# Performance work log

Hardware: AMD Instinct MI355X
Metric: run time of the kernel (lower is better)

## Reference

```python
import jax, jax.numpy as jnp
import numpy as np

N_NODES = 50000
N_EDGES = 1000000
D_IN = 64
D_OUT = 64
EDGE_DIM = 16
NEG_SLOPE = 0.2


def setup_inputs() -> dict:
    key = jax.random.key(0)
    ks = jax.random.split(key, 10)
    x = jax.random.normal(ks[0], (N_NODES, D_IN), dtype=jnp.float32)
    edge_index = jax.random.randint(ks[1], (2, N_EDGES), 0, N_NODES, dtype=jnp.int64)
    edge_attr = jax.random.normal(ks[2], (N_EDGES, EDGE_DIM), dtype=jnp.float32)
    s = 0.1
    W_l = jax.random.normal(ks[3], (D_IN, D_OUT), dtype=jnp.float32) * s
    b_l = jnp.zeros((D_OUT,), dtype=jnp.float32)
    W_r = jax.random.normal(ks[4], (D_IN, D_OUT), dtype=jnp.float32) * s
    b_r = jnp.zeros((D_OUT,), dtype=jnp.float32)
    W_e = jax.random.normal(ks[5], (EDGE_DIM, D_OUT), dtype=jnp.float32) * s
    att = jax.random.normal(ks[6], (D_OUT,), dtype=jnp.float32) * s
    bias = jnp.zeros((D_OUT,), dtype=jnp.float32)
    return {"x": x, "edge_index": edge_index, "edge_attr": edge_attr,
            "W_l": W_l, "b_l": b_l, "W_r": W_r, "b_r": b_r,
            "W_e": W_e, "att": att, "bias": bias}


def reference(x, edge_index, edge_attr, W_l, b_l, W_r, b_r, W_e, att, bias):
    # GATv2Conv (heads=1, concat) with edge features, share_weights=False.
    src = edge_index[0]  # message source j
    dst = edge_index[1]  # aggregation target i
    n = x.shape[0]

    x_l = x @ W_l + b_l          # [N, C] source transform
    x_r = x @ W_r + b_r          # [N, C] target transform
    e = edge_attr @ W_e          # [E, C] edge transform (no bias in lin_edge)

    # per-edge GATv2 attention logit: a^T LeakyReLU(x_l[j] + x_r[i] + e)
    h = jax.nn.leaky_relu(x_l[src] + x_r[dst] + e, NEG_SLOPE)  # [E, C]
    logits = h @ att  # [E]

    # segment softmax over incoming edges of each target node
    m = jax.ops.segment_max(logits, dst, num_segments=n)        # [N]
    ex = jnp.exp(logits - m[dst])                               # [E]
    denom = jax.ops.segment_sum(ex, dst, num_segments=n)       # [N]
    alpha = ex / (denom[dst] + 1e-16)                           # [E]

    # weighted scatter-add of source messages x_l[j]
    out = jax.ops.segment_sum(alpha[:, None] * x_l[src], dst, num_segments=n)
    return out + bias
```

## Files before the change

### kernel.cpp

```cpp
#include <hip/hip_runtime.h>
#include <hip/hip_bf16.h>
#include <math.h>

#define N_NODES 50000
#define N_EDGES 1000000
#define D 64
#define ED 16
#define NEG 0.2f

__device__ __forceinline__ float wave_sum(float v) {
  #pragma unroll
  for (int m = 32; m >= 1; m >>= 1) v += __shfl_xor(v, m, 64);
  return v;
}

__global__ void k_init(int* __restrict__ cursor) {
  int i = blockIdx.x * 256 + threadIdx.x;
  if (i < N_NODES) cursor[i] = 0;
}

__global__ __launch_bounds__(256) void k_transform(
    const float* __restrict__ x,
    const float* __restrict__ Wl, const float* __restrict__ bl,
    const float* __restrict__ Wr, const float* __restrict__ br,
    __hip_bfloat16* __restrict__ xlb, float* __restrict__ xr) {
  __shared__ float sW[2 * D * D];
  float* sWl = sW;
  float* sWr = sW + D * D;
  int t = threadIdx.x;
  for (int q = t; q < D * D / 4; q += 256) {
    ((float4*)sWl)[q] = ((const float4*)Wl)[q];
    ((float4*)sWr)[q] = ((const float4*)Wr)[q];
  }
  __syncthreads();
  int lane = t & 63;
  int row = blockIdx.x * 4 + (t >> 6);
  if (row >= N_NODES) return;
  float xv = x[row * D + lane];
  float accl = bl[lane], accr = br[lane];
  #pragma unroll
  for (int k = 0; k < D; k++) {
    float xk = __shfl(xv, k, 64);
    accl = fmaf(xk, sWl[k * D + lane], accl);
    accr = fmaf(xk, sWr[k * D + lane], accr);
  }
  xlb[row * D + lane] = __float2bfloat16(accl);
  xr[row * D + lane] = accr;
}

__global__ void k_hist(const int* __restrict__ ei, int* __restrict__ cursor) {
  int e = blockIdx.x * 256 + threadIdx.x;
  if (e < N_EDGES) atomicAdd(&cursor[ei[N_EDGES + e]], 1);
}

__global__ void k_scan_a(const int* __restrict__ counts, int* __restrict__ row_start,
                         int* __restrict__ bsum) {
  __shared__ int sb[256];
  int t = threadIdx.x;
  int i = blockIdx.x * 256 + t;
  int v = (i < N_NODES) ? counts[i] : 0;
  sb[t] = v;
  __syncthreads();
  for (int off = 1; off < 256; off <<= 1) {
    int add = (t >= off) ? sb[t - off] : 0;
    __syncthreads();
    sb[t] += add;
    __syncthreads();
  }
  if (i < N_NODES) row_start[i] = sb[t] - v;
  if (t == 255) bsum[blockIdx.x] = sb[t];
}
__global__ void k_scan_b(int* __restrict__ bsum, int nb) {
  __shared__ int sb[256];
  int t = threadIdx.x;
  int v = (t < nb) ? bsum[t] : 0;
  sb[t] = v;
  __syncthreads();
  for (int off = 1; off < 256; off <<= 1) {
    int add = (t >= off) ? sb[t - off] : 0;
    __syncthreads();
    sb[t] += add;
    __syncthreads();
  }
  if (t < nb) bsum[t] = sb[t] - v;
}
__global__ void k_scan_c(int* __restrict__ row_start, const int* __restrict__ bsum,
                         int* __restrict__ cursor) {
  int t = threadIdx.x;
  int i = blockIdx.x * 256 + t;
  if (i < N_NODES) {
    int r = row_start[i] + bsum[blockIdx.x];
    row_start[i] = r;
    cursor[i] = r;
  }
  if (i == 0) row_start[N_NODES] = N_EDGES;
}

__global__ void k_scatter(const int* __restrict__ ei, int* __restrict__ cursor,
                          int2* __restrict__ perm) {
  int e = blockIdx.x * 256 + threadIdx.x;
  if (e >= N_EDGES) return;
  int s = ei[e];
  int d = ei[N_EDGES + e];
  int pos = atomicAdd(&cursor[d], 1);
  perm[pos] = make_int2(e, s);
}

__global__ __launch_bounds__(256) void k_fused(
    const float* __restrict__ ea, const float* __restrict__ We,
    const float* __restrict__ att,
    const __hip_bfloat16* __restrict__ xlb, const float* __restrict__ xr,
    const int* __restrict__ row_start, const int2* __restrict__ perm,
    const float* __restrict__ bias, float* __restrict__ out) {
  __shared__ float sWe[ED * D];
  __shared__ float satt[D];
  int t = threadIdx.x;
  for (int q = t; q < ED * D / 4; q += 256) ((float4*)sWe)[q] = ((const float4*)We)[q];
  if (t < D) satt[t] = att[t];
  __syncthreads();
  int lane = t & 63;
  int n = blockIdx.x * 4 + (t >> 6);
  if (n >= N_NODES) return;
  int start = row_start[n];
  int end = row_start[n + 1];

  float xrv = xr[(size_t)n * D + lane];
  float av = satt[lane];
  float m = -INFINITY, lsum = 0.f, O = 0.f;

  const unsigned short* xlr16 = (const unsigned short*)xlb;

  if (start < end) {
    int2 p0 = perm[start];
    int e0 = __builtin_amdgcn_readfirstlane(p0.x);
    int s0 = __builtin_amdgcn_readfirstlane(p0.y);
    unsigned short xlr = xlr16[(size_t)s0 * D + lane];
    float eav = (lane < ED) ? ea[(size_t)e0 * ED + lane] : 0.f;
    int i1 = (start + 1 < end) ? start + 1 : start;
    int2 pp = perm[i1];

    for (int i = start; i < end; ++i) {
      int e_n = __builtin_amdgcn_readfirstlane(pp.x);
      int s_n = __builtin_amdgcn_readfirstlane(pp.y);
      unsigned short xlr_n = xlr16[(size_t)s_n * D + lane];
      float eav_n = (lane < ED) ? ea[(size_t)e_n * ED + lane] : 0.f;
      int i2 = (i + 2 < end) ? i + 2 : i1;
      pp = perm[i2];

      float xlv = __uint_as_float(((unsigned)xlr) << 16);
      float acc = 0.f;
      #pragma unroll
      for (int k = 0; k < ED; k++) {
        float ek = __shfl(eav, k, 64);
        acc = fmaf(ek, sWe[k * D + lane], acc);
      }
      float h = xlv + xrv + acc;
      h = (h > 0.f) ? h : NEG * h;
      float logit = wave_sum(h * av);
      float mn = fmaxf(m, logit);
      float sc = __expf(m - mn);
      float p = __expf(logit - mn);
      lsum = fmaf(lsum, sc, p);
      O = O * sc + p * xlv;
      m = mn;
      xlr = xlr_n;
      eav = eav_n;
    }
  }
  out[(size_t)n * D + lane] = O / (lsum + 1e-16f) + bias[lane];
}

static inline char* align_up(char* p, size_t a) {
  return (char*)(((uintptr_t)p + a - 1) & ~(uintptr_t)(a - 1));
}

extern "C" void kernel_launch(void* const* d_in, const int* in_sizes, int n_in,
                              void* d_out, int out_size, void* d_ws, size_t ws_size,
                              hipStream_t stream) {
  const float* x   = (const float*)d_in[0];
  const int* ei    = (const int*)d_in[1];
  const float* ea  = (const float*)d_in[2];
  const float* Wl  = (const float*)d_in[3];
  const float* bl  = (const float*)d_in[4];
  const float* Wr  = (const float*)d_in[5];
  const float* br  = (const float*)d_in[6];
  const float* We  = (const float*)d_in[7];
  const float* att = (const float*)d_in[8];
  const float* bias = (const float*)d_in[9];
  float* out = (float*)d_out;

  char* w = (char*)d_ws;
  __hip_bfloat16* xlb = (__hip_bfloat16*)w; w = align_up(w + (size_t)N_NODES * D * 2, 256);
  float* xr       = (float*)w; w = align_up(w + (size_t)N_NODES * D * 4, 256);
  int* row_start  = (int*)w;   w = align_up(w + (size_t)(N_NODES + 1) * 4, 256);
  int* cursor     = (int*)w;   w = align_up(w + (size_t)N_NODES * 4, 256);
  int* bsum       = (int*)w;   w = align_up(w + 256 * 4, 256);
  int2* perm      = (int2*)w;  w = align_up(w + (size_t)N_EDGES * 8, 256);

  const int NB = (N_NODES + 255) / 256;

  k_init<<<NB, 256, 0, stream>>>(cursor);
  k_transform<<<N_NODES / 4, 256, 0, stream>>>(x, Wl, bl, Wr, br, xlb, xr);
  k_hist<<<(N_EDGES + 255) / 256, 256, 0, stream>>>(ei, cursor);
  k_scan_a<<<NB, 256, 0, stream>>>(cursor, row_start, bsum);
  k_scan_b<<<1, 256, 0, stream>>>(bsum, NB);
  k_scan_c<<<NB, 256, 0, stream>>>(row_start, bsum, cursor);
  k_scatter<<<(N_EDGES + 255) / 256, 256, 0, stream>>>(ei, cursor, perm);
  k_fused<<<(N_NODES + 3) / 4, 256, 0, stream>>>(ea, We, att, xlb, xr, row_start,
                                                 perm, bias, out);
}
```

Before: 537.4 us.

## Pre-permute edge attributes into CSR order as bf16 during scatter

The scatter kernel now reads each edge's 16 float attributes and writes them as bf16 into dst-sorted CSR order alongside a source-only permutation array. The fused kernel then reads edge attributes contiguously instead of gathering random 64-byte rows by edge id, and reads only 4-byte source indices. This removes random gathers from the main aggregation loop in exchange for an extra 32MB write plus read, and bf16 rounding of edge attributes. The init kernel is also replaced by hipMemsetAsync.

```diff
diff --git a/kernel.cpp b/kernel.cpp
--- a/kernel.cpp
+++ b/kernel.cpp
@@ -14,9 +14,12 @@
   return v;
 }
 
-__global__ void k_init(int* __restrict__ cursor) {
-  int i = blockIdx.x * 256 + threadIdx.x;
-  if (i < N_NODES) cursor[i] = 0;
+__device__ __forceinline__ unsigned short f2bf(float x) {
+  __hip_bfloat16 h = __float2bfloat16(x);
+  return *(unsigned short*)&h;
+}
+__device__ __forceinline__ float bf2f(unsigned short u) {
+  return __uint_as_float(((unsigned)u) << 16);
 }
 
 __global__ __launch_bounds__(256) void k_transform(
@@ -97,20 +100,37 @@
 }
 
 __global__ void k_scatter(const int* __restrict__ ei, int* __restrict__ cursor,
-                          int2* __restrict__ perm) {
+                          int* __restrict__ src_perm, uint4* __restrict__ eap,
+                          const float* __restrict__ ea) {
   int e = blockIdx.x * 256 + threadIdx.x;
   if (e >= N_EDGES) return;
   int s = ei[e];
   int d = ei[N_EDGES + e];
+  const float4* ea4 = (const float4*)ea;
+  float4 a = ea4[(size_t)e * 4 + 0];
+  float4 b = ea4[(size_t)e * 4 + 1];
+  float4 c = ea4[(size_t)e * 4 + 2];
+  float4 f = ea4[(size_t)e * 4 + 3];
   int pos = atomicAdd(&cursor[d], 1);
-  perm[pos] = make_int2(e, s);
+  src_perm[pos] = s;
+  uint4 w0, w1;
+  w0.x = (unsigned)f2bf(a.x) | ((unsigned)f2bf(a.y) << 16);
+  w0.y = (unsigned)f2bf(a.z) | ((unsigned)f2bf(a.w) << 16);
+  w0.z = (unsigned)f2bf(b.x) | ((unsigned)f2bf(b.y) << 16);
+  w0.w = (unsigned)f2bf(b.z) | ((unsigned)f2bf(b.w) << 16);
+  w1.x = (unsigned)f2bf(c.x) | ((unsigned)f2bf(c.y) << 16);
+  w1.y = (unsigned)f2bf(c.z) | ((unsigned)f2bf(c.w) << 16);
+  w1.z = (unsigned)f2bf(f.x) | ((unsigned)f2bf(f.y) << 16);
+  w1.w = (unsigned)f2bf(f.z) | ((unsigned)f2bf(f.w) << 16);
+  eap[(size_t)pos * 2 + 0] = w0;
+  eap[(size_t)pos * 2 + 1] = w1;
 }
 
 __global__ __launch_bounds__(256) void k_fused(
-    const float* __restrict__ ea, const float* __restrict__ We,
+    const unsigned short* __restrict__ eap, const float* __restrict__ We,
     const float* __restrict__ att,
     const __hip_bfloat16* __restrict__ xlb, const float* __restrict__ xr,
-    const int* __restrict__ row_start, const int2* __restrict__ perm,
+    const int* __restrict__ row_start, const int* __restrict__ src_perm,
     const float* __restrict__ bias, float* __restrict__ out) {
   __shared__ float sWe[ED * D];
   __shared__ float satt[D];
@@ -131,27 +151,26 @@
   const unsigned short* xlr16 = (const unsigned short*)xlb;
 
   if (start < end) {
-    int2 p0 = perm[start];
-    int e0 = __builtin_amdgcn_readfirstlane(p0.x);
-    int s0 = __builtin_amdgcn_readfirstlane(p0.y);
+    int s0 = __builtin_amdgcn_readfirstlane(src_perm[start]);
     unsigned short xlr = xlr16[(size_t)s0 * D + lane];
-    float eav = (lane < ED) ? ea[(size_t)e0 * ED + lane] : 0.f;
+    unsigned short ear = (lane < ED) ? eap[(size_t)start * ED + lane] : 0;
     int i1 = (start + 1 < end) ? start + 1 : start;
-    int2 pp = perm[i1];
+    int sp = src_perm[i1];
 
     for (int i = start; i < end; ++i) {
-      int e_n = __builtin_amdgcn_readfirstlane(pp.x);
-      int s_n = __builtin_amdgcn_readfirstlane(pp.y);
+      int s_n = __builtin_amdgcn_readfirstlane(sp);
       unsigned short xlr_n = xlr16[(size_t)s_n * D + lane];
-      float eav_n = (lane < ED) ? ea[(size_t)e_n * ED + lane] : 0.f;
+      int inext = (i + 1 < end) ? i + 1 : i;
+      unsigned short ear_n = (lane < ED) ? eap[(size_t)inext * ED + lane] : 0;
       int i2 = (i + 2 < end) ? i + 2 : i1;
-      pp = perm[i2];
-
-      float xlv = __uint_as_float(((unsigned)xlr) << 16);
+      sp = src_perm[i2];
+
+      float xlv = bf2f(xlr);
+      float eavf = bf2f(ear);
       float acc = 0.f;
       #pragma unroll
       for (int k = 0; k < ED; k++) {
-        float ek = __shfl(eav, k, 64);
+        float ek = __shfl(eavf, k, 64);
         acc = fmaf(ek, sWe[k * D + lane], acc);
       }
       float h = xlv + xrv + acc;
@@ -164,7 +183,7 @@
       O = O * sc + p * xlv;
       m = mn;
       xlr = xlr_n;
-      eav = eav_n;
+      ear = ear_n;
     }
   }
   out[(size_t)n * D + lane] = O / (lsum + 1e-16f) + bias[lane];
@@ -195,17 +214,18 @@
   int* row_start  = (int*)w;   w = align_up(w + (size_t)(N_NODES + 1) * 4, 256);
   int* cursor     = (int*)w;   w = align_up(w + (size_t)N_NODES * 4, 256);
   int* bsum       = (int*)w;   w = align_up(w + 256 * 4, 256);
-  int2* perm      = (int2*)w;  w = align_up(w + (size_t)N_EDGES * 8, 256);
+  int* src_perm   = (int*)w;   w = align_up(w + (size_t)N_EDGES * 4, 256);
+  uint4* eap      = (uint4*)w; w = align_up(w + (size_t)N_EDGES * ED * 2, 256);
 
   const int NB = (N_NODES + 255) / 256;
 
-  k_init<<<NB, 256, 0, stream>>>(cursor);
+  hipMemsetAsync(cursor, 0, (size_t)N_NODES * 4, stream);
   k_transform<<<N_NODES / 4, 256, 0, stream>>>(x, Wl, bl, Wr, br, xlb, xr);
   k_hist<<<(N_EDGES + 255) / 256, 256, 0, stream>>>(ei, cursor);
   k_scan_a<<<NB, 256, 0, stream>>>(cursor, row_start, bsum);
   k_scan_b<<<1, 256, 0, stream>>>(bsum, NB);
   k_scan_c<<<NB, 256, 0, stream>>>(row_start, bsum, cursor);
-  k_scatter<<<(N_EDGES + 255) / 256, 256, 0, stream>>>(ei, cursor, perm);
-  k_fused<<<(N_NODES + 3) / 4, 256, 0, stream>>>(ea, We, att, xlb, xr, row_start,
-                                                 perm, bias, out);
-}
+  k_scatter<<<(N_EDGES + 255) / 256, 256, 0, stream>>>(ei, cursor, src_perm, eap, ea);
+  k_fused<<<(N_NODES + 3) / 4, 256, 0, stream>>>((const unsigned short*)eap, We, att,
+                                                 xlb, xr, row_start, src_perm, bias, out);
+}
```

Result: no change. 528.9 us (-1.6%).
